# Kernel optimization log

Hardware: AMD Instinct MI355X
Metric: run time of the kernel (lower is better)

The kernel has to match this reference:

```python
import jax, jax.numpy as jnp
import numpy as np

HIDDEN_DIM = 1024
NUM_HEADS = 8
CONTEXT_LEN = 8
HEAD_DIM = HIDDEN_DIM // NUM_HEADS


def setup_inputs() -> dict:
    key = jax.random.key(0)
    ks = jax.random.split(key, 6)
    B, C, H, W = 32, HIDDEN_DIM, 18, 32
    K = CONTEXT_LEN
    h_current = jax.random.normal(ks[0], (B, C, H, W), dtype=jnp.float32)
    h_buffer = jax.random.normal(ks[1], (K, B, C, H, W), dtype=jnp.float32)
    # Parameters (torch nn.Linear stores weight as [out, in]; y = x @ W.T + b)
    s_qkv = 1.0 / np.sqrt(C)
    W_qkv = jax.random.uniform(ks[2], (3 * C, C), jnp.float32, -s_qkv, s_qkv)
    W_out = jax.random.uniform(ks[3], (C, C), jnp.float32, -s_qkv, s_qkv)
    b_out = jax.random.uniform(ks[4], (C,), jnp.float32, -s_qkv, s_qkv)
    rel_emb = jax.random.normal(ks[5], (2 * CONTEXT_LEN + 1, NUM_HEADS), dtype=jnp.float32)
    return {"h_current": h_current, "h_buffer": h_buffer, "W_qkv": W_qkv,
            "W_out": W_out, "b_out": b_out, "rel_emb": rel_emb}


def reference(h_current, h_buffer, W_qkv, W_out, b_out, rel_emb):
    B, C, H, W = h_current.shape
    K = h_buffer.shape[0]
    T = K + 1
    nh, hd = NUM_HEADS, HEAD_DIM

    # spatial pooling (AdaptiveAvgPool2d(1)) then stack buffer frames + current
    pooled_buf = h_buffer.mean(axis=(3, 4))          # [K, B, C]
    pooled_cur = h_current.mean(axis=(2, 3))         # [B, C]
    context = jnp.concatenate(
        [jnp.transpose(pooled_buf, (1, 0, 2)), pooled_cur[:, None, :]], axis=1)  # [B, T, C]

    # QKV projection (no bias)
    qkv = context @ W_qkv.T                          # [B, T, 3C]
    q, k, v = jnp.split(qkv, 3, axis=-1)
    q = q.reshape(B, T, nh, hd).transpose(0, 2, 1, 3)  # [B, nh, T, hd]
    k = k.reshape(B, T, nh, hd).transpose(0, 2, 1, 3)
    v = v.reshape(B, T, nh, hd).transpose(0, 2, 1, 3)

    # relative-position bias
    idx = jnp.arange(T)
    rel = jnp.clip(idx[:, None] - idx[None, :], -CONTEXT_LEN, CONTEXT_LEN) + CONTEXT_LEN
    bias = rel_emb[rel]                              # [T, T, nh]
    bias = jnp.transpose(bias, (2, 0, 1))            # [nh, T, T]

    # causal mask (-inf above diagonal) combined with bias
    causal = jnp.triu(jnp.full((T, T), -jnp.inf, dtype=context.dtype), k=1)
    attn_mask = causal[None, None, :, :] + bias[None, :, :, :]  # [1, nh, T, T]

    scale = 1.0 / np.sqrt(hd)
    scores = jnp.einsum('bhqd,bhkd->bhqk', q, k) * scale + attn_mask
    attn = jax.nn.softmax(scores, axis=-1)
    attn_out = jnp.einsum('bhqk,bhkd->bhqd', attn, v)  # [B, nh, T, hd]
    attn_out = attn_out.transpose(0, 2, 1, 3).reshape(B, T, C)

    # output projection of final timestep, broadcast over spatial dims, residual
    out = attn_out[:, -1] @ W_out.T + b_out          # [B, C]
    return h_current + out[:, :, None, None]
```

## Files before the change

### kernel.cpp

```cpp
#include <hip/hip_runtime.h>
#include <hip/hip_bf16.h>

#define BB 32
#define CC 1024
#define HWSZ 576
#define KCTX 8
#define TT 9
#define NH 8
#define HD 128

#define GBM 32
#define GBN 128
#define GBK 32

#define NS_KV 4
#define NS_Q  8
#define NS_O  32

#define KV_MN (288 * 2048)
#define Q_MN  (32 * 1024)

typedef float v4f __attribute__((ext_vector_type(4)));

__global__ __launch_bounds__(256) void pool_kernel(
    const float* __restrict__ hbuf,
    const float* __restrict__ hcur,
    float* __restrict__ ctx)
{
    const int wave = threadIdx.x >> 6;
    const int lane = threadIdx.x & 63;
    const int stride = gridDim.x * 4;
    const int nrows = BB * TT * CC;

    for (int r = blockIdx.x * 4 + wave; r < nrows; r += stride) {
        float sum;
        int cidx;
        if (r < KCTX * BB * CC) {
            const v4f* s4 = (const v4f*)(hbuf + (size_t)r * HWSZ);
            const int t = r >> 15;
            const int b = (r >> 10) & 31;
            const int c = r & (CC - 1);
            cidx = (b * TT + t) * CC + c;
            v4f v0 = __builtin_nontemporal_load(s4 + lane);
            v4f v1 = __builtin_nontemporal_load(s4 + lane + 64);
            sum = v0.x + v0.y + v0.z + v0.w + v1.x + v1.y + v1.z + v1.w;
            if (lane < 16) {
                v4f v2 = __builtin_nontemporal_load(s4 + lane + 128);
                sum += v2.x + v2.y + v2.z + v2.w;
            }
        } else {
            const int rc = r - KCTX * BB * CC;
            const v4f* s4 = (const v4f*)(hcur + (size_t)rc * HWSZ);
            const int b = rc >> 10;
            const int c = rc & (CC - 1);
            cidx = (b * TT + KCTX) * CC + c;
            v4f v0 = s4[lane];
            v4f v1 = s4[lane + 64];
            sum = v0.x + v0.y + v0.z + v0.w + v1.x + v1.y + v1.z + v1.w;
            if (lane < 16) {
                v4f v2 = s4[lane + 128];
                sum += v2.x + v2.y + v2.z + v2.w;
            }
        }
#pragma unroll
        for (int off = 32; off; off >>= 1) sum += __shfl_xor(sum, off);
        if (lane == 0) ctx[cidx] = sum * (1.0f / 576.0f);
    }
}

template <int ES>
__device__ __forceinline__ void gemm_tile_body(
    const float* __restrict__ Ablk, int lda,
    const float* __restrict__ Bblk, int ldb,
    float* __restrict__ Yout, int ldy,
    int k0, int klen,
    float (*As)[GBK + 4], float (*Bs)[GBN + 4])
{
    const int tid = threadIdx.x;
    const int tx = tid & 15;
    const int ty = tid >> 4;

    float acc0[8], acc1[8];
#pragma unroll
    for (int i = 0; i < 8; ++i) { acc0[i] = 0.f; acc1[i] = 0.f; }

    for (int kt = k0; kt < k0 + klen; kt += GBK) {
        {
            const int row = tid >> 3;
            const int kc = (tid & 7) << 2;
            float4 a = *(const float4*)(Ablk + (size_t)row * lda + kt + kc);
            *(float4*)(&As[row][kc]) = a;
        }
        {
            const int kc = (tid & 7) << 2;
            const int r0 = tid >> 3;
#pragma unroll
            for (int rr = 0; rr < 4; ++rr) {
                const int row = r0 + rr * 32;
                float4 bv = *(const float4*)(Bblk + (size_t)row * ldb + kt + kc);
                Bs[kc + 0][row] = bv.x;
                Bs[kc + 1][row] = bv.y;
                Bs[kc + 2][row] = bv.z;
                Bs[kc + 3][row] = bv.w;
            }
        }
        __syncthreads();

#pragma unroll
        for (int k4 = 0; k4 < GBK; k4 += 4) {
            float4 a0 = *(const float4*)(&As[ty * 2 + 0][k4]);
            float4 a1 = *(const float4*)(&As[ty * 2 + 1][k4]);
            const float a0v[4] = {a0.x, a0.y, a0.z, a0.w};
            const float a1v[4] = {a1.x, a1.y, a1.z, a1.w};
#pragma unroll
            for (int i = 0; i < 4; ++i) {
                float4 blo = *(const float4*)(&Bs[k4 + i][tx * 8]);
                float4 bhi = *(const float4*)(&Bs[k4 + i][tx * 8 + 4]);
                acc0[0] += a0v[i] * blo.x;  acc0[1] += a0v[i] * blo.y;
                acc0[2] += a0v[i] * blo.z;  acc0[3] += a0v[i] * blo.w;
                acc0[4] += a0v[i] * bhi.x;  acc0[5] += a0v[i] * bhi.y;
                acc0[6] += a0v[i] * bhi.z;  acc0[7] += a0v[i] * bhi.w;
                acc1[0] += a1v[i] * blo.x;  acc1[1] += a1v[i] * blo.y;
                acc1[2] += a1v[i] * blo.z;  acc1[3] += a1v[i] * blo.w;
                acc1[4] += a1v[i] * bhi.x;  acc1[5] += a1v[i] * bhi.y;
                acc1[6] += a1v[i] * bhi.z;  acc1[7] += a1v[i] * bhi.w;
            }
        }
        __syncthreads();
    }

    const int col = tx * 8;
    const int row0 = ty * 2;
    if (ES == 1) {
        float* y0 = Yout + (size_t)row0 * ldy + col;
        float* y1 = y0 + ldy;
        *(float4*)(y0 + 0) = make_float4(acc0[0], acc0[1], acc0[2], acc0[3]);
        *(float4*)(y0 + 4) = make_float4(acc0[4], acc0[5], acc0[6], acc0[7]);
        *(float4*)(y1 + 0) = make_float4(acc1[0], acc1[1], acc1[2], acc1[3]);
        *(float4*)(y1 + 4) = make_float4(acc1[4], acc1[5], acc1[6], acc1[7]);
    } else {
        float* y0 = Yout + (size_t)row0 * ldy;
        float* y1 = y0 + ldy;
#pragma unroll
        for (int i = 0; i < 8; ++i) {
            y0[(size_t)(col + i) * ES] = acc0[i];
            y1[(size_t)(col + i) * ES] = acc1[i];
        }
    }
}

__global__ __launch_bounds__(256) void qkv_gemm(
    const float* __restrict__ ctx, const float* __restrict__ Wqkv,
    float* __restrict__ qpart, float* __restrict__ kvpart)
{
    __shared__ float As[GBM][GBK + 4];
    __shared__ float Bs[GBK][GBN + 4];

    const int bid = blockIdx.x;
    if (bid < NS_Q * 8) {
        const int s = bid & (NS_Q - 1);
        const int bn = bid >> 3;
        gemm_tile_body<1>(ctx + 8 * CC, TT * CC,
                          Wqkv + (size_t)bn * GBN * CC, CC,
                          qpart + (size_t)s * Q_MN + bn * GBN, 1024,
                          s * (1024 / NS_Q), 1024 / NS_Q, As, Bs);
    } else {
        const int rel = bid - NS_Q * 8;
        const int s = rel & (NS_KV - 1);
        const int tile = rel >> 2;
        const int bm = tile >> 4;
        const int bn = tile & 15;
        gemm_tile_body<1>(ctx + (size_t)bm * GBM * CC, CC,
                          Wqkv + (size_t)CC * CC + (size_t)bn * GBN * CC, CC,
                          kvpart + (size_t)s * KV_MN + (size_t)bm * GBM * 2048 + bn * GBN, 2048,
                          s * (1024 / NS_KV), 1024 / NS_KV, As, Bs);
    }
}

__global__ __launch_bounds__(64) void attn_kernel(
    const float* __restrict__ kvpart,
    const float* __restrict__ qpart,
    const float* __restrict__ rel_emb,
    float* __restrict__ attn_out)
{
    const int lane = threadIdx.x;
    const int pair = blockIdx.x;
    const int b = pair >> 3;
    const int h = pair & 7;
    const float scale = 0.08838834764831845f;

    const int qoff = b * CC + h * HD;
    float q1 = 0.f, q2 = 0.f;
#pragma unroll
    for (int s = 0; s < NS_Q; ++s) {
        q1 += qpart[(size_t)s * Q_MN + qoff + lane];
        q2 += qpart[(size_t)s * Q_MN + qoff + lane + 64];
    }
    q1 *= scale; q2 *= scale;

    float sc[TT];
#pragma unroll
    for (int j = 0; j < TT; ++j) {
        const size_t base = (size_t)(b * TT + j) * 2048 + h * HD;
        float k1 = 0.f, k2 = 0.f;
#pragma unroll
        for (int s = 0; s < NS_KV; ++s) {
            k1 += kvpart[(size_t)s * KV_MN + base + lane];
            k2 += kvpart[(size_t)s * KV_MN + base + lane + 64];
        }
        float p = q1 * k1 + q2 * k2;
#pragma unroll
        for (int off = 32; off; off >>= 1) p += __shfl_xor(p, off);
        sc[j] = p + rel_emb[(2 * KCTX - j) * NH + h];
    }
    float m = sc[0];
#pragma unroll
    for (int j = 1; j < TT; ++j) m = fmaxf(m, sc[j]);
    float sum = 0.f;
#pragma unroll
    for (int j = 0; j < TT; ++j) { sc[j] = expf(sc[j] - m); sum += sc[j]; }
    const float inv = 1.0f / sum;

    float a1 = 0.f, a2 = 0.f;
#pragma unroll
    for (int j = 0; j < TT; ++j) {
        const size_t base = (size_t)(b * TT + j) * 2048 + 1024 + h * HD;
        float v1 = 0.f, v2 = 0.f;
#pragma unroll
        for (int s = 0; s < NS_KV; ++s) {
            v1 += kvpart[(size_t)s * KV_MN + base + lane];
            v2 += kvpart[(size_t)s * KV_MN + base + lane + 64];
        }
        a1 += sc[j] * v1;
        a2 += sc[j] * v2;
    }
    attn_out[qoff + lane] = a1 * inv;
    attn_out[qoff + lane + 64] = a2 * inv;
}

__global__ __launch_bounds__(256) void out_gemm(
    const float* __restrict__ attnb, const float* __restrict__ Wout,
    float* __restrict__ outpart)
{
    __shared__ float As[GBM][GBK + 4];
    __shared__ float Bs[GBK][GBN + 4];
    const int s = blockIdx.x & (NS_O - 1);
    const int bn = blockIdx.x >> 5;
    gemm_tile_body<NS_O>(attnb, 1024,
                         Wout + (size_t)bn * GBN * CC, CC,
                         outpart + (size_t)bn * GBN * NS_O + s, 1024 * NS_O,
                         s * (1024 / NS_O), 1024 / NS_O, As, Bs);
}

__global__ __launch_bounds__(256) void final_bcast(
    const float* __restrict__ hc,
    const float* __restrict__ outpart,
    const float* __restrict__ bias,
    float* __restrict__ y)
{
    const int wave = threadIdx.x >> 6;
    const int lane = threadIdx.x & 63;
    const int stride = gridDim.x * 4;
    const int nrows = BB * CC;

    for (int r = blockIdx.x * 4 + wave; r < nrows; r += stride) {
        const int c = r & (CC - 1);
        v4f p4 = *((const v4f*)(outpart + (size_t)r * NS_O) + (lane & 7));
        float p = p4.x + p4.y + p4.z + p4.w;
        p += __shfl_xor(p, 1);
        p += __shfl_xor(p, 2);
        p += __shfl_xor(p, 4);
        const float add = p + bias[c];

        const v4f* s4 = (const v4f*)(hc + (size_t)r * HWSZ);
        v4f* d4 = (v4f*)(y + (size_t)r * HWSZ);
        v4f v0 = s4[lane];
        v0.x += add; v0.y += add; v0.z += add; v0.w += add;
        __builtin_nontemporal_store(v0, d4 + lane);
        v4f v1 = s4[lane + 64];
        v1.x += add; v1.y += add; v1.z += add; v1.w += add;
        __builtin_nontemporal_store(v1, d4 + lane + 64);
        if (lane < 16) {
            v4f v2 = s4[lane + 128];
            v2.x += add; v2.y += add; v2.z += add; v2.w += add;
            __builtin_nontemporal_store(v2, d4 + lane + 128);
        }
    }
}

extern "C" void kernel_launch(void* const* d_in, const int* in_sizes, int n_in,
                              void* d_out, int out_size, void* d_ws, size_t ws_size,
                              hipStream_t stream) {
    const float* h_current = (const float*)d_in[0];
    const float* h_buffer  = (const float*)d_in[1];
    const float* W_qkv     = (const float*)d_in[2];
    const float* W_out     = (const float*)d_in[3];
    const float* b_out     = (const float*)d_in[4];
    const float* rel_emb   = (const float*)d_in[5];

    float* ws = (float*)d_ws;
    float* ctx     = ws;
    float* kvpart  = ctx + 294912;
    float* qpart   = kvpart + (size_t)NS_KV * KV_MN;
    float* attnb   = qpart + (size_t)NS_Q * Q_MN;
    float* outpart = attnb + 32768;

    pool_kernel<<<2048, 256, 0, stream>>>(h_buffer, h_current, ctx);

    qkv_gemm<<<NS_Q * 8 + NS_KV * 144, 256, 0, stream>>>(ctx, W_qkv, qpart, kvpart);

    attn_kernel<<<BB * NH, 64, 0, stream>>>(kvpart, qpart, rel_emb, attnb);

    out_gemm<<<8 * NS_O, 256, 0, stream>>>(attnb, W_out, outpart);

    final_bcast<<<2048, 256, 0, stream>>>(h_current, outpart, b_out, (float*)d_out);
}
```

Before: 179.7 us.

## Fuse output projection into broadcast kernel, repack pooling rows, widen KV split-K

The separate output-projection GEMM and its partial-sum buffer are removed. Each wave in the final broadcast kernel now computes its own dot product of the attention row with a W_out row before adding to h_current. The pooling kernel now reduces four rows per wave, using 16 lanes per row and nine vector loads, which cuts shuffle work and raises memory-level parallelism. The KV split-K factor is doubled to 8, giving more blocks at the cost of a larger partial buffer and more reads in the attention kernel. Fusing drops one launch, but W_out rows are re-read once per batch (32 times) from cache.

```diff
diff --git a/kernel.cpp b/kernel.cpp
--- a/kernel.cpp
+++ b/kernel.cpp
@@ -13,9 +13,8 @@
 #define GBN 128
 #define GBK 32
 
-#define NS_KV 4
+#define NS_KV 8
 #define NS_Q  8
-#define NS_O  32
 
 #define KV_MN (288 * 2048)
 #define Q_MN  (32 * 1024)
@@ -29,46 +28,40 @@
 {
     const int wave = threadIdx.x >> 6;
     const int lane = threadIdx.x & 63;
-    const int stride = gridDim.x * 4;
+    const int sub  = lane >> 4;
+    const int l16  = lane & 15;
+    const int stride = gridDim.x * 16;
     const int nrows = BB * TT * CC;
 
-    for (int r = blockIdx.x * 4 + wave; r < nrows; r += stride) {
-        float sum;
+    for (int r0 = (blockIdx.x * 4 + wave) * 4; r0 < nrows; r0 += stride) {
+        const int r = r0 + sub;
+        v4f acc = {0.f, 0.f, 0.f, 0.f};
         int cidx;
         if (r < KCTX * BB * CC) {
             const v4f* s4 = (const v4f*)(hbuf + (size_t)r * HWSZ);
             const int t = r >> 15;
             const int b = (r >> 10) & 31;
-            const int c = r & (CC - 1);
-            cidx = (b * TT + t) * CC + c;
-            v4f v0 = __builtin_nontemporal_load(s4 + lane);
-            v4f v1 = __builtin_nontemporal_load(s4 + lane + 64);
-            sum = v0.x + v0.y + v0.z + v0.w + v1.x + v1.y + v1.z + v1.w;
-            if (lane < 16) {
-                v4f v2 = __builtin_nontemporal_load(s4 + lane + 128);
-                sum += v2.x + v2.y + v2.z + v2.w;
-            }
+            cidx = (b * TT + t) * CC + (r & (CC - 1));
+#pragma unroll
+            for (int j = 0; j < 9; ++j)
+                acc += __builtin_nontemporal_load(s4 + l16 + 16 * j);
         } else {
             const int rc = r - KCTX * BB * CC;
             const v4f* s4 = (const v4f*)(hcur + (size_t)rc * HWSZ);
-            const int b = rc >> 10;
-            const int c = rc & (CC - 1);
-            cidx = (b * TT + KCTX) * CC + c;
-            v4f v0 = s4[lane];
-            v4f v1 = s4[lane + 64];
-            sum = v0.x + v0.y + v0.z + v0.w + v1.x + v1.y + v1.z + v1.w;
-            if (lane < 16) {
-                v4f v2 = s4[lane + 128];
-                sum += v2.x + v2.y + v2.z + v2.w;
-            }
-        }
-#pragma unroll
-        for (int off = 32; off; off >>= 1) sum += __shfl_xor(sum, off);
-        if (lane == 0) ctx[cidx] = sum * (1.0f / 576.0f);
-    }
-}
-
-template <int ES>
+            cidx = ((rc >> 10) * TT + KCTX) * CC + (rc & (CC - 1));
+#pragma unroll
+            for (int j = 0; j < 9; ++j)
+                acc += s4[l16 + 16 * j];
+        }
+        float sum = acc.x + acc.y + acc.z + acc.w;
+        sum += __shfl_xor(sum, 1);
+        sum += __shfl_xor(sum, 2);
+        sum += __shfl_xor(sum, 4);
+        sum += __shfl_xor(sum, 8);
+        if (l16 == 0) ctx[cidx] = sum * (1.0f / 576.0f);
+    }
+}
+
 __device__ __forceinline__ void gemm_tile_body(
     const float* __restrict__ Ablk, int lda,
     const float* __restrict__ Bblk, int ldb,
@@ -131,22 +124,12 @@
 
     const int col = tx * 8;
     const int row0 = ty * 2;
-    if (ES == 1) {
-        float* y0 = Yout + (size_t)row0 * ldy + col;
-        float* y1 = y0 + ldy;
-        *(float4*)(y0 + 0) = make_float4(acc0[0], acc0[1], acc0[2], acc0[3]);
-        *(float4*)(y0 + 4) = make_float4(acc0[4], acc0[5], acc0[6], acc0[7]);
-        *(float4*)(y1 + 0) = make_float4(acc1[0], acc1[1], acc1[2], acc1[3]);
-        *(float4*)(y1 + 4) = make_float4(acc1[4], acc1[5], acc1[6], acc1[7]);
-    } else {
-        float* y0 = Yout + (size_t)row0 * ldy;
-        float* y1 = y0 + ldy;
-#pragma unroll
-        for (int i = 0; i < 8; ++i) {
-            y0[(size_t)(col + i) * ES] = acc0[i];
-            y1[(size_t)(col + i) * ES] = acc1[i];
-        }
-    }
+    float* y0 = Yout + (size_t)row0 * ldy + col;
+    float* y1 = y0 + ldy;
+    *(float4*)(y0 + 0) = make_float4(acc0[0], acc0[1], acc0[2], acc0[3]);
+    *(float4*)(y0 + 4) = make_float4(acc0[4], acc0[5], acc0[6], acc0[7]);
+    *(float4*)(y1 + 0) = make_float4(acc1[0], acc1[1], acc1[2], acc1[3]);
+    *(float4*)(y1 + 4) = make_float4(acc1[4], acc1[5], acc1[6], acc1[7]);
 }
 
 __global__ __launch_bounds__(256) void qkv_gemm(
@@ -160,20 +143,20 @@
     if (bid < NS_Q * 8) {
         const int s = bid & (NS_Q - 1);
         const int bn = bid >> 3;
-        gemm_tile_body<1>(ctx + 8 * CC, TT * CC,
-                          Wqkv + (size_t)bn * GBN * CC, CC,
-                          qpart + (size_t)s * Q_MN + bn * GBN, 1024,
-                          s * (1024 / NS_Q), 1024 / NS_Q, As, Bs);
+        gemm_tile_body(ctx + 8 * CC, TT * CC,
+                       Wqkv + (size_t)bn * GBN * CC, CC,
+                       qpart + (size_t)s * Q_MN + bn * GBN, 1024,
+                       s * (1024 / NS_Q), 1024 / NS_Q, As, Bs);
     } else {
         const int rel = bid - NS_Q * 8;
         const int s = rel & (NS_KV - 1);
-        const int tile = rel >> 2;
+        const int tile = rel >> 3;
         const int bm = tile >> 4;
         const int bn = tile & 15;
-        gemm_tile_body<1>(ctx + (size_t)bm * GBM * CC, CC,
-                          Wqkv + (size_t)CC * CC + (size_t)bn * GBN * CC, CC,
-                          kvpart + (size_t)s * KV_MN + (size_t)bm * GBM * 2048 + bn * GBN, 2048,
-                          s * (1024 / NS_KV), 1024 / NS_KV, As, Bs);
+        gemm_tile_body(ctx + (size_t)bm * GBM * CC, CC,
+                       Wqkv + (size_t)CC * CC + (size_t)bn * GBN * CC, CC,
+                       kvpart + (size_t)s * KV_MN + (size_t)bm * GBM * 2048 + bn * GBN, 2048,
+                       s * (1024 / NS_KV), 1024 / NS_KV, As, Bs);
     }
 }
 
@@ -238,23 +221,10 @@
     attn_out[qoff + lane + 64] = a2 * inv;
 }
 
-__global__ __launch_bounds__(256) void out_gemm(
-    const float* __restrict__ attnb, const float* __restrict__ Wout,
-    float* __restrict__ outpart)
-{
-    __shared__ float As[GBM][GBK + 4];
-    __shared__ float Bs[GBK][GBN + 4];
-    const int s = blockIdx.x & (NS_O - 1);
-    const int bn = blockIdx.x >> 5;
-    gemm_tile_body<NS_O>(attnb, 1024,
-                         Wout + (size_t)bn * GBN * CC, CC,
-                         outpart + (size_t)bn * GBN * NS_O + s, 1024 * NS_O,
-                         s * (1024 / NS_O), 1024 / NS_O, As, Bs);
-}
-
-__global__ __launch_bounds__(256) void final_bcast(
+__global__ __launch_bounds__(256) void final_fused(
     const float* __restrict__ hc,
-    const float* __restrict__ outpart,
+    const float* __restrict__ attnb,
+    const float* __restrict__ Wout,
     const float* __restrict__ bias,
     float* __restrict__ y)
 {
@@ -264,13 +234,22 @@
     const int nrows = BB * CC;
 
     for (int r = blockIdx.x * 4 + wave; r < nrows; r += stride) {
+        const int b = r >> 10;
         const int c = r & (CC - 1);
-        v4f p4 = *((const v4f*)(outpart + (size_t)r * NS_O) + (lane & 7));
-        float p = p4.x + p4.y + p4.z + p4.w;
-        p += __shfl_xor(p, 1);
-        p += __shfl_xor(p, 2);
-        p += __shfl_xor(p, 4);
-        const float add = p + bias[c];
+
+        const v4f* ar = (const v4f*)(attnb + (size_t)b * CC);
+        const v4f* wr = (const v4f*)(Wout + (size_t)c * CC);
+        v4f acc = {0.f, 0.f, 0.f, 0.f};
+#pragma unroll
+        for (int j = 0; j < 4; ++j) {
+            v4f a = ar[lane + 64 * j];
+            v4f w = wr[lane + 64 * j];
+            acc += a * w;
+        }
+        float dot = acc.x + acc.y + acc.z + acc.w;
+#pragma unroll
+        for (int off = 32; off; off >>= 1) dot += __shfl_xor(dot, off);
+        const float add = dot + bias[c];
 
         const v4f* s4 = (const v4f*)(hc + (size_t)r * HWSZ);
         v4f* d4 = (v4f*)(y + (size_t)r * HWSZ);
@@ -299,11 +278,10 @@
     const float* rel_emb   = (const float*)d_in[5];
 
     float* ws = (float*)d_ws;
-    float* ctx     = ws;
-    float* kvpart  = ctx + 294912;
-    float* qpart   = kvpart + (size_t)NS_KV * KV_MN;
-    float* attnb   = qpart + (size_t)NS_Q * Q_MN;
-    float* outpart = attnb + 32768;
+    float* ctx    = ws;
+    float* kvpart = ctx + 294912;
+    float* qpart  = kvpart + (size_t)NS_KV * KV_MN;
+    float* attnb  = qpart + (size_t)NS_Q * Q_MN;
 
     pool_kernel<<<2048, 256, 0, stream>>>(h_buffer, h_current, ctx);
 
@@ -311,7 +289,5 @@
 
     attn_kernel<<<BB * NH, 64, 0, stream>>>(kvpart, qpart, rel_emb, attnb);
 
-    out_gemm<<<8 * NS_O, 256, 0, stream>>>(attnb, W_out, outpart);
-
-    final_bcast<<<2048, 256, 0, stream>>>(h_current, outpart, b_out, (float*)d_out);
-}
+    final_fused<<<2048, 256, 0, stream>>>(h_current, attnb, W_out, b_out, (float*)d_out);
+}
```

Measured after the change: 165.1 us. 8.1% less time.
